# Kernel optimization log

Hardware: AMD Instinct MI355X
Metric: run time of the kernel (lower is better)

The kernel has to match this reference:

```python
import jax, jax.numpy as jnp
import numpy as np

N = 50000      # nodes
E = 800000     # edges
H = 128        # hidden_channels
EC = 50        # edge_channels
NF = 128       # num_filters
TC = 128       # time_channels
CUTOFF = 0.8


def ssp(x):
    # ShiftedSoftplus: softplus(x) - log(2)
    return jax.nn.softplus(x) - jnp.log(2.0)


def setup_inputs() -> dict:
    key = jax.random.key(0)
    ks = jax.random.split(key, 24)

    def xavier(k, shape):
        fan_in, fan_out = shape
        s = float(np.sqrt(6.0 / (fan_in + fan_out)))
        return jax.random.uniform(k, shape, minval=-s, maxval=s, dtype=jnp.float32)

    return {
        "tt": jax.random.uniform(ks[0], (N, 1), dtype=jnp.float32),
        "xx": jax.random.normal(ks[1], (N, H), dtype=jnp.float32),
        "edge_index": jax.random.randint(ks[2], (2, E), 0, N, dtype=jnp.int64),
        "edge_length": jax.random.uniform(ks[3], (E, 1), dtype=jnp.float32),
        "edge_attr": jax.random.normal(ks[4], (E, EC), dtype=jnp.float32),
        # shared edge MLP (same module instance used by conv1 and conv2)
        "em1_w": xavier(ks[5], (EC, NF)),
        "em1_b": jnp.zeros((NF,), jnp.float32),
        "em2_w": xavier(ks[6], (NF, NF)),
        "em2_b": jnp.zeros((NF,), jnp.float32),
        # conv1
        "c1_m1w": xavier(ks[7], (H, NF)),
        "c1_m2w": xavier(ks[8], (NF, H)),
        "c1_m2b": jnp.zeros((H,), jnp.float32),
        # conv2
        "c2_m1w": xavier(ks[9], (H, NF)),
        "c2_m2w": xavier(ks[10], (NF, H)),
        "c2_m2b": jnp.zeros((H,), jnp.float32),
        # time embedding projection
        "te_w": xavier(ks[11], (TC, H)),
        "te_b": jnp.zeros((H,), jnp.float32),
        # final linear
        "lin_w": xavier(ks[12], (H, H)),
        "lin_b": jnp.zeros((H,), jnp.float32),
    }


def reference(tt, xx, edge_index, edge_length, edge_attr,
              em1_w, em1_b, em2_w, em2_b,
              c1_m1w, c1_m2w, c1_m2b,
              c2_m1w, c2_m2w, c2_m2b,
              te_w, te_b, lin_w, lin_b):
    src, dst = edge_index[0], edge_index[1]  # message: x_j = x[src], aggregate at dst

    # smooth cutoff weight C: [E,1]
    C = 0.5 * (jnp.cos(edge_length * jnp.pi / CUTOFF) + 1.0)
    C = C * (edge_length <= CUTOFF) * (edge_length >= 0.0)

    # shared edge MLP filter, cutoff-weighted: [E,NF]
    Wf = ssp(edge_attr @ em1_w + em1_b) @ em2_w + em2_b
    Wf = Wf * C

    def cfconv(x, m1w, m2w, m2b):
        msg = (x @ m1w)[src] * Wf                         # gather-multiply [E,NF]
        agg = jax.ops.segment_sum(msg, dst, num_segments=N)  # scatter-add [N,NF]
        return agg @ m2w + m2b

    x = cfconv(xx, c1_m1w, c1_m2w, c1_m2b)

    # sinusoidal time embedding -> swish -> proj
    half = TC // 2
    coef = jnp.exp(jnp.arange(half, dtype=jnp.float32) * (-np.log(1000.0) / (half - 1)))
    e = tt * coef[None, :]
    e = jnp.concatenate([jnp.sin(e), jnp.cos(e)], axis=-1)  # [N,TC]
    t = (e * jax.nn.sigmoid(e)) @ te_w + te_b

    x = ssp(x + t)
    x = cfconv(x, c2_m1w, c2_m2w, c2_m2b)
    x = ssp(x)
    x = ssp(x @ lin_w + lin_b)
    return x
```

## Files before the change

### kernel.cpp

```cpp
#include <hip/hip_runtime.h>
#include <hip/hip_bf16.h>
#include <math.h>

#define NF 128
#define EC 50
#define ET 64
#define SCH 2048
#define CUTOFF 0.8f
#define PI_F 3.14159265358979323846f

typedef __attribute__((ext_vector_type(8))) _Float16 f16x8;
typedef __attribute__((ext_vector_type(2))) _Float16 f16x2;
typedef __attribute__((ext_vector_type(4))) float f32x4;

__device__ __forceinline__ float4 ld4(const float* p) { return *reinterpret_cast<const float4*>(p); }

__device__ __forceinline__ float sspf(float x) {
    return fmaxf(x, 0.0f) + __logf(1.0f + __expf(-fabsf(x))) - 0.69314718055994530942f;
}
__device__ __forceinline__ float swishf(float x) {
    return x / (1.0f + __expf(-x));
}

__global__ __launch_bounds__(256) void emb_kernel(const float* __restrict__ tt,
                                                  float* __restrict__ emb, int n) {
    int i = blockIdx.x * blockDim.x + threadIdx.x;
    if (i >= n * 64) return;
    int node = i >> 6, k = i & 63;
    float t = tt[node];
    float coef = __expf((float)k * (-6.9077552789821368f / 63.0f));
    float e = t * coef;
    emb[node * NF + k]      = swishf(__sinf(e));
    emb[node * NF + 64 + k] = swishf(__cosf(e));
}

template<int MODE>
__global__ void mfma_gemm(const float* A,
                          const float* __restrict__ W,
                          const float* __restrict__ bias,
                          const float* extra,
                          float* out, int n) {
    __shared__ __align__(16) char A_lds[64 * 256];
    const int tid  = threadIdx.x;
    const int wid  = tid >> 6;
    const int lane = tid & 63;
    const int l15  = lane & 15;
    const int lhi  = lane >> 4;

    f16x8 wfr[2][4];
    float bc[2];
    #pragma unroll
    for (int ct = 0; ct < 2; ct++) {
        const int col = (2 * wid + ct) * 16 + l15;
        bc[ct] = (MODE != 0) ? bias[col] : 0.0f;
        #pragma unroll
        for (int t = 0; t < 4; t++)
            #pragma unroll
            for (int j = 0; j < 8; j++) {
                int k = t * 32 + lhi * 8 + j;
                wfr[ct][t][j] = (_Float16)W[k * NF + col];
            }
    }

    const int ntile = (n + 63) >> 6;
    for (int tile = blockIdx.x; tile < ntile; tile += gridDim.x) {
        const int base = tile << 6;
        __syncthreads();
        {
            int row = tid >> 2, part = tid & 3;
            int grow = base + row;
            bool val = grow < n;
            const float* ap = A + (size_t)grow * NF + part * 32;
            #pragma unroll
            for (int kk = 0; kk < 32; kk += 4) {
                float4 v = val ? ld4(ap + kk) : make_float4(0.f, 0.f, 0.f, 0.f);
                int k = part * 32 + kk;
                f16x2 p0; p0[0] = (_Float16)v.x; p0[1] = (_Float16)v.y;
                f16x2 p1; p1[0] = (_Float16)v.z; p1[1] = (_Float16)v.w;
                *(f16x2*)(A_lds + row * 256 + ((2 * k)       ^ ((row & 7) << 4))) = p0;
                *(f16x2*)(A_lds + row * 256 + ((2 * (k + 2)) ^ ((row & 7) << 4))) = p1;
            }
        }
        __syncthreads();

        f32x4 acc[4][2];
        #pragma unroll
        for (int m = 0; m < 4; m++) {
            #pragma unroll
            for (int ct = 0; ct < 2; ct++) {
                f32x4 b = {bc[ct], bc[ct], bc[ct], bc[ct]};
                acc[m][ct] = b;
            }
            const int row = m * 16 + l15;
            #pragma unroll
            for (int t2 = 0; t2 < 4; t2++) {
                int o = row * 256 + ((t2 * 64 + lhi * 16) ^ ((row & 7) << 4));
                f16x8 a = *(const f16x8*)(A_lds + o);
                #pragma unroll
                for (int ct = 0; ct < 2; ct++)
                    acc[m][ct] = __builtin_amdgcn_mfma_f32_16x16x32_f16(a, wfr[ct][t2], acc[m][ct], 0, 0, 0);
            }
        }

        #pragma unroll
        for (int m = 0; m < 4; m++) {
            #pragma unroll
            for (int ct = 0; ct < 2; ct++) {
                const int col = (2 * wid + ct) * 16 + l15;
                #pragma unroll
                for (int r = 0; r < 4; r++) {
                    int grow = base + m * 16 + lhi * 4 + r;
                    if (grow >= n) continue;
                    float v = acc[m][ct][r];
                    if (MODE == 2) v += extra[(size_t)grow * NF + col];
                    if (MODE == 1 || MODE == 2) v = sspf(v);
                    out[(size_t)grow * NF + col] = v;
                }
            }
        }
    }
}

__global__ __launch_bounds__(256) void deg_kernel(const int* __restrict__ ei,
                                                  int* __restrict__ deg, int E_) {
    int e = blockIdx.x * blockDim.x + threadIdx.x;
    if (e < E_) atomicAdd(&deg[ei[E_ + e]], 1);
}

__global__ __launch_bounds__(256) void scan_chunk(const int* __restrict__ deg,
                                                  int* __restrict__ csum, int n) {
    int base = blockIdx.x * SCH;
    int s = 0;
    for (int i = threadIdx.x; i < SCH; i += 256) {
        int idx = base + i;
        if (idx < n) s += deg[idx];
    }
    __shared__ int red[4];
    #pragma unroll
    for (int d = 1; d < 64; d <<= 1) s += __shfl_xor(s, d);
    if ((threadIdx.x & 63) == 0) red[threadIdx.x >> 6] = s;
    __syncthreads();
    if (threadIdx.x == 0) csum[blockIdx.x] = red[0] + red[1] + red[2] + red[3];
}

__global__ __launch_bounds__(1024) void scan_csum_k(const int* __restrict__ csum,
                                                    int* __restrict__ coff, int nch,
                                                    int* __restrict__ off, int n, int E_) {
    __shared__ int sm[1024];
    const int tid = threadIdx.x;
    int v = (tid < nch) ? csum[tid] : 0;
    sm[tid] = v;
    __syncthreads();
    for (int st = 1; st < 1024; st <<= 1) {
        int t = (tid >= st) ? sm[tid - st] : 0;
        __syncthreads();
        sm[tid] += t;
        __syncthreads();
    }
    if (tid < nch) coff[tid] = sm[tid] - v;
    if (tid == 0) off[n] = E_;
}

__global__ __launch_bounds__(256) void scan_emit(const int* __restrict__ deg,
                                                 const int* __restrict__ coff,
                                                 int* __restrict__ off, int n) {
    const int base = blockIdx.x * SCH + threadIdx.x * 8;
    int vals[8]; int s = 0;
    #pragma unroll
    for (int j = 0; j < 8; j++) {
        int idx = base + j;
        vals[j] = (idx < n) ? deg[idx] : 0;
        s += vals[j];
    }
    __shared__ int ts[256];
    ts[threadIdx.x] = s;
    __syncthreads();
    for (int st = 1; st < 256; st <<= 1) {
        int t = (threadIdx.x >= st) ? ts[threadIdx.x - st] : 0;
        __syncthreads();
        ts[threadIdx.x] += t;
        __syncthreads();
    }
    int prefix = coff[blockIdx.x] + ts[threadIdx.x] - s;
    #pragma unroll
    for (int j = 0; j < 8; j++) {
        int idx = base + j;
        if (idx < n) off[idx] = prefix;
        prefix += vals[j];
    }
}

__global__ __launch_bounds__(256) void scatter_kernel(const int* __restrict__ ei,
                                                      const float* __restrict__ elen,
                                                      const int* __restrict__ off,
                                                      int* __restrict__ cur,
                                                      int* __restrict__ perm,
                                                      int* __restrict__ srcp,
                                                      float* __restrict__ Cp, int E_) {
    int e = blockIdx.x * blockDim.x + threadIdx.x;
    if (e < E_) {
        int d = ei[E_ + e];
        int p = off[d] + atomicAdd(&cur[d], 1);
        perm[p] = e;
        srcp[p] = ei[e];
        float len = elen[e];
        float c = 0.5f * (__cosf(len * (PI_F / CUTOFF)) + 1.0f);
        Cp[p] = (len <= CUTOFF && len >= 0.0f) ? c : 0.0f;
    }
}

__global__ __launch_bounds__(256) void tilebnd_kernel(const int* __restrict__ off,
                                                      int* __restrict__ tnlo,
                                                      int nN, int ntiles) {
    int t = blockIdx.x * blockDim.x + threadIdx.x;
    if (t > ntiles) return;
    if (t == ntiles) { tnlo[t] = nN; return; }
    int key = t * ET;
    int lo = 0, hi = nN + 1;
    while (lo < hi) { int mid = (lo + hi) >> 1; if (off[mid] < key) lo = mid + 1; else hi = mid; }
    tnlo[t] = lo;
}

__global__ __launch_bounds__(256, 3) void wf_kernel(const float* __restrict__ eattr,
                                                    const float* __restrict__ em1w,
                                                    const float* __restrict__ em1b,
                                                    const float* __restrict__ em2w,
                                                    const float* __restrict__ em2b,
                                                    const int* __restrict__ perm,
                                                    const float* __restrict__ Cp,
                                                    unsigned int* __restrict__ wmsg32,
                                                    int E_) {
    __shared__ __align__(16) char U[ET * 128 + ET * 256];
    __shared__ float C_sm[ET];
    char* ea_p  = U;
    char* h_p   = U + ET * 128;
    char* msg_b = U;

    const int tid  = threadIdx.x;
    const int wid  = tid >> 6;
    const int lane = tid & 63;
    const int l15  = lane & 15;
    const int lhi  = lane >> 4;

    f16x8 w1f[2][2];
    f16x8 w2f[2][4];
    float b1c[2], b2c[2];
    #pragma unroll
    for (int ct = 0; ct < 2; ct++) {
        const int col = (2 * wid + ct) * 16 + l15;
        b1c[ct] = em1b[col];
        b2c[ct] = em2b[col];
        #pragma unroll
        for (int t = 0; t < 2; t++)
            #pragma unroll
            for (int j = 0; j < 8; j++) {
                int k = t * 32 + lhi * 8 + j;
                w1f[ct][t][j] = (_Float16)((k < EC) ? em1w[k * NF + col] : 0.0f);
            }
        #pragma unroll
        for (int t = 0; t < 4; t++)
            #pragma unroll
            for (int j = 0; j < 8; j++) {
                int k = t * 32 + lhi * 8 + j;
                w2f[ct][t][j] = (_Float16)em2w[k * NF + col];
            }
    }

    const int ntiles = (E_ + ET - 1) / ET;
    for (int tile = blockIdx.x; tile < ntiles; tile += gridDim.x) {
        const int base = tile * ET;
        const int ec = min(ET, E_ - base);
        const int mmax = (ec + 15) >> 4;
        __syncthreads();

        if (tid < ET) C_sm[tid] = (tid < ec) ? Cp[base + tid] : 0.0f;
        {
            int row = tid >> 2, part = tid & 3;
            bool val = row < ec;
            const float* ep = eattr + (size_t)(val ? perm[base + row] : 0) * EC;
            #pragma unroll
            for (int kk = 0; kk < 16; kk += 2) {
                int k = part * 16 + kk;
                float2 v = make_float2(0.f, 0.f);
                if (val && k <= 48) v = *(const float2*)(ep + k);
                f16x2 pk;
                pk[0] = (_Float16)v.x; pk[1] = (_Float16)v.y;
                *(f16x2*)(ea_p + row * 128 + ((2 * k) ^ ((row & 7) << 4))) = pk;
            }
        }
        __syncthreads();

        f32x4 acc[4][2];
        #pragma unroll
        for (int m = 0; m < 4; m++) {
            if (m < mmax) {
                #pragma unroll
                for (int ct = 0; ct < 2; ct++) {
                    f32x4 b = {b1c[ct], b1c[ct], b1c[ct], b1c[ct]};
                    acc[m][ct] = b;
                }
                const int row = m * 16 + l15;
                #pragma unroll
                for (int t1 = 0; t1 < 2; t1++) {
                    int o = row * 128 + ((t1 * 64 + lhi * 16) ^ ((row & 7) << 4));
                    f16x8 a = *(const f16x8*)(ea_p + o);
                    #pragma unroll
                    for (int ct = 0; ct < 2; ct++)
                        acc[m][ct] = __builtin_amdgcn_mfma_f32_16x16x32_f16(a, w1f[ct][t1], acc[m][ct], 0, 0, 0);
                }
            }
        }
        #pragma unroll
        for (int m = 0; m < 4; m++) {
            if (m < mmax) {
                #pragma unroll
                for (int ct = 0; ct < 2; ct++) {
                    const int col = (2 * wid + ct) * 16 + l15;
                    #pragma unroll
                    for (int r = 0; r < 4; r++) {
                        int row = m * 16 + lhi * 4 + r;
                        *(_Float16*)(h_p + row * 256 + ((2 * col) ^ ((row & 7) << 4))) =
                            (_Float16)sspf(acc[m][ct][r]);
                    }
                }
            }
        }
        __syncthreads();

        #pragma unroll
        for (int m = 0; m < 4; m++) {
            if (m < mmax) {
                #pragma unroll
                for (int ct = 0; ct < 2; ct++) {
                    f32x4 b = {b2c[ct], b2c[ct], b2c[ct], b2c[ct]};
                    acc[m][ct] = b;
                }
                const int row = m * 16 + l15;
                #pragma unroll
                for (int t2 = 0; t2 < 4; t2++) {
                    int o = row * 256 + ((t2 * 64 + lhi * 16) ^ ((row & 7) << 4));
                    f16x8 a = *(const f16x8*)(h_p + o);
                    #pragma unroll
                    for (int ct = 0; ct < 2; ct++)
                        acc[m][ct] = __builtin_amdgcn_mfma_f32_16x16x32_f16(a, w2f[ct][t2], acc[m][ct], 0, 0, 0);
                }
            }
        }
        __syncthreads();

        #pragma unroll
        for (int m = 0; m < 4; m++) {
            if (m < mmax) {
                #pragma unroll
                for (int ct = 0; ct < 2; ct++) {
                    #pragma unroll
                    for (int r = 0; r < 4; r++) {
                        int e = m * 16 + lhi * 4 + r;
                        int ch = (2 * wid + ct) * 16 + l15;
                        *(_Float16*)(msg_b + e * 264 + 2 * ch) =
                            (_Float16)(acc[m][ct][r] * C_sm[e]);
                    }
                }
            }
        }
        __syncthreads();

        for (int j = tid; j < ec * 64; j += 256)
            __builtin_nontemporal_store(
                *(const unsigned int*)(msg_b + (j >> 6) * 264 + (j & 63) * 4),
                &wmsg32[(size_t)base * 64 + j]);
    }
}

__global__ __launch_bounds__(256) void red_conv(const float* __restrict__ y,
                                                const unsigned int* __restrict__ wmsg32,
                                                const int* __restrict__ srcp,
                                                const int* __restrict__ off,
                                                const int* __restrict__ tnlo,
                                                float* __restrict__ agg,
                                                int ntiles) {
    const int wid  = threadIdx.x >> 6;
    const int lane = threadIdx.x & 63;
    const int c2   = lane * 2;

    for (int tile = blockIdx.x; tile < ntiles; tile += gridDim.x) {
        const int n_lo = tnlo[tile], n_hi1 = tnlo[tile + 1];
        for (int n = n_lo + wid; n < n_hi1; n += 4) {
            float2 a = make_float2(0.f, 0.f);
            int i = off[n];
            const int e1 = off[n + 1];
            for (; i + 4 <= e1; i += 4) {
                int s0 = srcp[i], s1 = srcp[i + 1], s2 = srcp[i + 2], s3 = srcp[i + 3];
                unsigned int u0 = __builtin_nontemporal_load(&wmsg32[(size_t)(i    ) * 64 + lane]);
                unsigned int u1 = __builtin_nontemporal_load(&wmsg32[(size_t)(i + 1) * 64 + lane]);
                unsigned int u2 = __builtin_nontemporal_load(&wmsg32[(size_t)(i + 2) * 64 + lane]);
                unsigned int u3 = __builtin_nontemporal_load(&wmsg32[(size_t)(i + 3) * 64 + lane]);
                float2 y0 = *(const float2*)(y + (size_t)s0 * NF + c2);
                float2 y1 = *(const float2*)(y + (size_t)s1 * NF + c2);
                float2 y2 = *(const float2*)(y + (size_t)s2 * NF + c2);
                float2 y3 = *(const float2*)(y + (size_t)s3 * NF + c2);
                f16x2 m0 = *(const f16x2*)&u0, m1 = *(const f16x2*)&u1;
                f16x2 m2 = *(const f16x2*)&u2, m3 = *(const f16x2*)&u3;
                a.x = fmaf((float)m0[0], y0.x, a.x); a.y = fmaf((float)m0[1], y0.y, a.y);
                a.x = fmaf((float)m1[0], y1.x, a.x); a.y = fmaf((float)m1[1], y1.y, a.y);
                a.x = fmaf((float)m2[0], y2.x, a.x); a.y = fmaf((float)m2[1], y2.y, a.y);
                a.x = fmaf((float)m3[0], y3.x, a.x); a.y = fmaf((float)m3[1], y3.y, a.y);
            }
            for (; i < e1; i++) {
                unsigned int u = __builtin_nontemporal_load(&wmsg32[(size_t)i * 64 + lane]);
                f16x2 mp = *(const f16x2*)&u;
                float2 yv = *(const float2*)(y + (size_t)srcp[i] * NF + c2);
                a.x = fmaf((float)mp[0], yv.x, a.x);
                a.y = fmaf((float)mp[1], yv.y, a.y);
            }
            *(float2*)(agg + (size_t)n * NF + c2) = a;
        }
    }
}

extern "C" void kernel_launch(void* const* d_in, const int* in_sizes, int n_in,
                              void* d_out, int out_size, void* d_ws, size_t ws_size,
                              hipStream_t stream) {
    const float* tt    = (const float*)d_in[0];
    const float* xx    = (const float*)d_in[1];
    const int*   ei    = (const int*)d_in[2];
    const float* elen  = (const float*)d_in[3];
    const float* eattr = (const float*)d_in[4];
    const float* em1w  = (const float*)d_in[5];
    const float* em1b  = (const float*)d_in[6];
    const float* em2w  = (const float*)d_in[7];
    const float* em2b  = (const float*)d_in[8];
    const float* c1m1w = (const float*)d_in[9];
    const float* c1m2w = (const float*)d_in[10];
    const float* c1m2b = (const float*)d_in[11];
    const float* c2m1w = (const float*)d_in[12];
    const float* c2m2w = (const float*)d_in[13];
    const float* c2m2b = (const float*)d_in[14];
    const float* tew   = (const float*)d_in[15];
    const float* teb   = (const float*)d_in[16];
    const float* linw  = (const float*)d_in[17];
    const float* linb  = (const float*)d_in[18];

    const int n  = in_sizes[0];
    const int E_ = in_sizes[2] / 2;
    const int ntiles = (E_ + ET - 1) / ET;
    const int gtiles = (n + 63) >> 6;
    const int nch = (n + SCH - 1) / SCH;
    float* out = (float*)d_out;

    const size_t NB = (size_t)n * NF;
    float* B0 = (float*)d_ws;
    float* B1 = B0 + NB;
    float* B2 = B1 + NB;
    int* off  = (int*)(B2 + NB);
    int* perm = off + (n + 1);
    int* deg  = perm + E_;
    int* cur  = deg + n;
    int* srcp = cur + n;
    int* tnlo = srcp + E_;
    int* csum = tnlo + ntiles + 1;
    int* coff = csum + nch;
    float* Cp = (float*)(coff + nch);
    unsigned int* wmsg32 = (unsigned int*)(Cp + E_);

    hipMemsetAsync(deg, 0, (size_t)2 * n * sizeof(int), stream);
    deg_kernel<<<(E_ + 255) / 256, 256, 0, stream>>>(ei, deg, E_);
    scan_chunk<<<nch, 256, 0, stream>>>(deg, csum, n);
    scan_csum_k<<<1, 1024, 0, stream>>>(csum, coff, nch, off, n, E_);
    scan_emit<<<nch, 256, 0, stream>>>(deg, coff, off, n);
    scatter_kernel<<<(E_ + 255) / 256, 256, 0, stream>>>(ei, elen, off, cur,
                                                         perm, srcp, Cp, E_);
    tilebnd_kernel<<<(ntiles + 256) / 256, 256, 0, stream>>>(off, tnlo, n, ntiles);

    emb_kernel<<<(n * 64 + 255) / 256, 256, 0, stream>>>(tt, B2, n);
    mfma_gemm<3><<<gtiles, 256, 0, stream>>>(B2, tew, teb, nullptr, B2, n);

    wf_kernel<<<2048, 256, 0, stream>>>(eattr, em1w, em1b, em2w, em2b,
                                        perm, Cp, wmsg32, E_);

    mfma_gemm<0><<<gtiles, 256, 0, stream>>>(xx, c1m1w, nullptr, nullptr, B0, n);

    red_conv<<<4096, 256, 0, stream>>>(B0, wmsg32, srcp, off, tnlo, B1, ntiles);

    mfma_gemm<2><<<gtiles, 256, 0, stream>>>(B1, c1m2w, c1m2b, B2, B2, n);

    mfma_gemm<0><<<gtiles, 256, 0, stream>>>(B2, c2m1w, nullptr, nullptr, B0, n);

    red_conv<<<4096, 256, 0, stream>>>(B0, wmsg32, srcp, off, tnlo, B1, ntiles);

    mfma_gemm<1><<<gtiles, 256, 0, stream>>>(B1, c2m2w, c2m2b, nullptr, B0, n);
    mfma_gemm<1><<<gtiles, 256, 0, stream>>>(B0, linw, linb, nullptr, out, n);
}
```

Baseline: 636.0 us.

## Split wf_kernel work across 8 waves with one column tile each

The edge-filter MLP kernel moves from 256-thread blocks, where each wave computes two 16-column tiles, to 512-thread blocks, where each of 8 waves computes a single 16-column tile. Per-thread register use for weights and accumulators halves, and the launch bounds now request more resident waves. The edge-attribute staging and output store loops are remapped to 512 threads, and the grid shrinks to 1280 blocks. The aim is higher occupancy and latency hiding, at the cost of each A-fragment load feeding only one MFMA instead of two.

```diff
diff --git a/kernel.cpp b/kernel.cpp
--- a/kernel.cpp
+++ b/kernel.cpp
@@ -221,7 +221,7 @@
     tnlo[t] = lo;
 }
 
-__global__ __launch_bounds__(256, 3) void wf_kernel(const float* __restrict__ eattr,
+__global__ __launch_bounds__(512, 4) void wf_kernel(const float* __restrict__ eattr,
                                                     const float* __restrict__ em1w,
                                                     const float* __restrict__ em1b,
                                                     const float* __restrict__ em2w,
@@ -241,30 +241,26 @@
     const int lane = tid & 63;
     const int l15  = lane & 15;
     const int lhi  = lane >> 4;
-
-    f16x8 w1f[2][2];
-    f16x8 w2f[2][4];
-    float b1c[2], b2c[2];
-    #pragma unroll
-    for (int ct = 0; ct < 2; ct++) {
-        const int col = (2 * wid + ct) * 16 + l15;
-        b1c[ct] = em1b[col];
-        b2c[ct] = em2b[col];
-        #pragma unroll
-        for (int t = 0; t < 2; t++)
-            #pragma unroll
-            for (int j = 0; j < 8; j++) {
-                int k = t * 32 + lhi * 8 + j;
-                w1f[ct][t][j] = (_Float16)((k < EC) ? em1w[k * NF + col] : 0.0f);
-            }
-        #pragma unroll
-        for (int t = 0; t < 4; t++)
-            #pragma unroll
-            for (int j = 0; j < 8; j++) {
-                int k = t * 32 + lhi * 8 + j;
-                w2f[ct][t][j] = (_Float16)em2w[k * NF + col];
-            }
-    }
+    const int col  = wid * 16 + l15;
+
+    f16x8 w1f[2];
+    f16x8 w2f[4];
+    const float b1c = em1b[col];
+    const float b2c = em2b[col];
+    #pragma unroll
+    for (int t = 0; t < 2; t++)
+        #pragma unroll
+        for (int j = 0; j < 8; j++) {
+            int k = t * 32 + lhi * 8 + j;
+            w1f[t][j] = (_Float16)((k < EC) ? em1w[k * NF + col] : 0.0f);
+        }
+    #pragma unroll
+    for (int t = 0; t < 4; t++)
+        #pragma unroll
+        for (int j = 0; j < 8; j++) {
+            int k = t * 32 + lhi * 8 + j;
+            w2f[t][j] = (_Float16)em2w[k * NF + col];
+        }
 
     const int ntiles = (E_ + ET - 1) / ET;
     for (int tile = blockIdx.x; tile < ntiles; tile += gridDim.x) {
@@ -275,12 +271,12 @@
 
         if (tid < ET) C_sm[tid] = (tid < ec) ? Cp[base + tid] : 0.0f;
         {
-            int row = tid >> 2, part = tid & 3;
+            int row = tid >> 3, part = tid & 7;
             bool val = row < ec;
             const float* ep = eattr + (size_t)(val ? perm[base + row] : 0) * EC;
             #pragma unroll
-            for (int kk = 0; kk < 16; kk += 2) {
-                int k = part * 16 + kk;
+            for (int kk = 0; kk < 8; kk += 2) {
+                int k = part * 8 + kk;
                 float2 v = make_float2(0.f, 0.f);
                 if (val && k <= 48) v = *(const float2*)(ep + k);
                 f16x2 pk;
@@ -290,23 +286,18 @@
         }
         __syncthreads();
 
-        f32x4 acc[4][2];
+        f32x4 acc[4];
         #pragma unroll
         for (int m = 0; m < 4; m++) {
             if (m < mmax) {
-                #pragma unroll
-                for (int ct = 0; ct < 2; ct++) {
-                    f32x4 b = {b1c[ct], b1c[ct], b1c[ct], b1c[ct]};
-                    acc[m][ct] = b;
-                }
+                f32x4 b = {b1c, b1c, b1c, b1c};
+                acc[m] = b;
                 const int row = m * 16 + l15;
                 #pragma unroll
                 for (int t1 = 0; t1 < 2; t1++) {
                     int o = row * 128 + ((t1 * 64 + lhi * 16) ^ ((row & 7) << 4));
                     f16x8 a = *(const f16x8*)(ea_p + o);
-                    #pragma unroll
-                    for (int ct = 0; ct < 2; ct++)
-                        acc[m][ct] = __builtin_amdgcn_mfma_f32_16x16x32_f16(a, w1f[ct][t1], acc[m][ct], 0, 0, 0);
+                    acc[m] = __builtin_amdgcn_mfma_f32_16x16x32_f16(a, w1f[t1], acc[m], 0, 0, 0);
                 }
             }
         }
@@ -314,14 +305,10 @@
         for (int m = 0; m < 4; m++) {
             if (m < mmax) {
                 #pragma unroll
-                for (int ct = 0; ct < 2; ct++) {
-                    const int col = (2 * wid + ct) * 16 + l15;
-                    #pragma unroll
-                    for (int r = 0; r < 4; r++) {
-                        int row = m * 16 + lhi * 4 + r;
-                        *(_Float16*)(h_p + row * 256 + ((2 * col) ^ ((row & 7) << 4))) =
-                            (_Float16)sspf(acc[m][ct][r]);
-                    }
+                for (int r = 0; r < 4; r++) {
+                    int row = m * 16 + lhi * 4 + r;
+                    *(_Float16*)(h_p + row * 256 + ((2 * col) ^ ((row & 7) << 4))) =
+                        (_Float16)sspf(acc[m][r]);
                 }
             }
         }
@@ -330,19 +317,14 @@
         #pragma unroll
         for (int m = 0; m < 4; m++) {
             if (m < mmax) {
-                #pragma unroll
-                for (int ct = 0; ct < 2; ct++) {
-                    f32x4 b = {b2c[ct], b2c[ct], b2c[ct], b2c[ct]};
-                    acc[m][ct] = b;
-                }
+                f32x4 b = {b2c, b2c, b2c, b2c};
+                acc[m] = b;
                 const int row = m * 16 + l15;
                 #pragma unroll
                 for (int t2 = 0; t2 < 4; t2++) {
                     int o = row * 256 + ((t2 * 64 + lhi * 16) ^ ((row & 7) << 4));
                     f16x8 a = *(const f16x8*)(h_p + o);
-                    #pragma unroll
-                    for (int ct = 0; ct < 2; ct++)
-                        acc[m][ct] = __builtin_amdgcn_mfma_f32_16x16x32_f16(a, w2f[ct][t2], acc[m][ct], 0, 0, 0);
+                    acc[m] = __builtin_amdgcn_mfma_f32_16x16x32_f16(a, w2f[t2], acc[m], 0, 0, 0);
                 }
             }
         }
@@ -352,20 +334,16 @@
         for (int m = 0; m < 4; m++) {
             if (m < mmax) {
                 #pragma unroll
-                for (int ct = 0; ct < 2; ct++) {
-                    #pragma unroll
-                    for (int r = 0; r < 4; r++) {
-                        int e = m * 16 + lhi * 4 + r;
-                        int ch = (2 * wid + ct) * 16 + l15;
-                        *(_Float16*)(msg_b + e * 264 + 2 * ch) =
-                            (_Float16)(acc[m][ct][r] * C_sm[e]);
-                    }
+                for (int r = 0; r < 4; r++) {
+                    int e = m * 16 + lhi * 4 + r;
+                    *(_Float16*)(msg_b + e * 264 + 2 * col) =
+                        (_Float16)(acc[m][r] * C_sm[e]);
                 }
             }
         }
         __syncthreads();
 
-        for (int j = tid; j < ec * 64; j += 256)
+        for (int j = tid; j < ec * 64; j += 512)
             __builtin_nontemporal_store(
                 *(const unsigned int*)(msg_b + (j >> 6) * 264 + (j & 63) * 4),
                 &wmsg32[(size_t)base * 64 + j]);
@@ -475,7 +453,7 @@
     emb_kernel<<<(n * 64 + 255) / 256, 256, 0, stream>>>(tt, B2, n);
     mfma_gemm<3><<<gtiles, 256, 0, stream>>>(B2, tew, teb, nullptr, B2, n);
 
-    wf_kernel<<<2048, 256, 0, stream>>>(eattr, em1w, em1b, em2w, em2b,
+    wf_kernel<<<1280, 512, 0, stream>>>(eattr, em1w, em1b, em2w, em2b,
                                         perm, Cp, wmsg32, E_);
 
     mfma_gemm<0><<<gtiles, 256, 0, stream>>>(xx, c1m1w, nullptr, nullptr, B0, n);
```

Measured after the change: 635.8 us. About the same (-0.0%).
